# Kernel optimization log

Hardware: AMD Instinct MI355X
Metric: run time of the kernel (lower is better)

## Reference

```python
import jax, jax.numpy as jnp
import numpy as np

PRE_NMS_THRESH = 0.05
PRE_NMS_TOP_N = 1000
NMS_THRESH = 0.6
POST_TOP_N = 100
MIN_SIZE = 0.0


def setup_inputs() -> dict:
    key = jax.random.key(0)
    k1, k2, k3 = jax.random.split(key, 3)
    N, C, H, W = 16, 80, 100, 152
    stride = 8.0
    xs = (jnp.arange(W, dtype=jnp.float32) + 0.5) * stride
    ys = (jnp.arange(H, dtype=jnp.float32) + 0.5) * stride
    yy, xx = jnp.meshgrid(ys, xs, indexing='ij')
    locations = jnp.stack([xx.reshape(-1), yy.reshape(-1)], axis=-1)  # [HW,2] (x,y)
    box_cls = jax.random.normal(k1, (N, C, H, W), jnp.float32) - 2.0  # logits
    box_regression = jax.random.uniform(k2, (N, 4, H, W), jnp.float32) * 64.0  # l,t,r,b >= 0
    centerness = jax.random.normal(k3, (N, 1, H, W), jnp.float32)
    image_sizes = jnp.tile(jnp.array([[800, 1216]], dtype=jnp.int32), (N, 1))  # (h, w)
    return {"locations": locations, "box_cls": box_cls, "box_regression": box_regression,
            "centerness": centerness, "image_sizes": image_sizes}


def _iou_matrix(b):  # b: [K,4] xyxy
    area = (b[:, 2] - b[:, 0]) * (b[:, 3] - b[:, 1])
    lt = jnp.maximum(b[:, None, :2], b[None, :, :2])
    rb = jnp.minimum(b[:, None, 2:], b[None, :, 2:])
    wh = jnp.clip(rb - lt, 0.0)
    inter = wh[..., 0] * wh[..., 1]
    return inter / (area[:, None] + area[None, :] - inter + 1e-9)


def _greedy_nms(iou, valid):  # boxes assumed sorted by score desc
    K = iou.shape[0]
    idx = jnp.arange(K)
    def body(i, sup):
        row = (iou[i] > NMS_THRESH) & (idx > i)
        return jnp.where(sup[i], sup, sup | row)
    sup = jax.lax.fori_loop(0, K, body, ~valid)
    return (~sup) & valid


def _forward(locations, box_cls, box_regression, centerness, image_sizes):
    N, C, H, W = box_cls.shape
    HW = H * W
    cls = jax.nn.sigmoid(jnp.transpose(box_cls, (0, 2, 3, 1)).reshape(N, HW, C))
    reg = jnp.transpose(box_regression, (0, 2, 3, 1)).reshape(N, HW, 4)
    ctr = jax.nn.sigmoid(jnp.transpose(centerness, (0, 2, 3, 1)).reshape(N, HW))
    cand = cls > PRE_NMS_THRESH
    scores = cls * ctr[:, :, None]
    flat = jnp.where(cand, scores, -jnp.inf).reshape(N, HW * C)
    top_scores, top_idx = jax.lax.top_k(flat, PRE_NMS_TOP_N)  # sorted desc
    loc_idx = top_idx // C
    labels = top_idx % C + 1
    valid = top_scores > -jnp.inf
    ar = jnp.arange(N)[:, None]
    reg_k = reg[ar, loc_idx]      # [N,K,4]
    loc_k = locations[loc_idx]    # [N,K,2]
    x1 = loc_k[..., 0] - reg_k[..., 0]
    y1 = loc_k[..., 1] - reg_k[..., 1]
    x2 = loc_k[..., 0] + reg_k[..., 2]
    y2 = loc_k[..., 1] + reg_k[..., 3]
    hi = image_sizes[:, 0:1].astype(x1.dtype)
    wi = image_sizes[:, 1:2].astype(x1.dtype)
    x1 = jnp.clip(x1, 0.0, wi - 1.0); x2 = jnp.clip(x2, 0.0, wi - 1.0)
    y1 = jnp.clip(y1, 0.0, hi - 1.0); y2 = jnp.clip(y2, 0.0, hi - 1.0)
    valid = valid & (x2 - x1 >= MIN_SIZE) & (y2 - y1 >= MIN_SIZE)
    sc = jnp.where(valid, jnp.sqrt(jnp.where(valid, top_scores, 1.0)), 0.0)
    boxes = jnp.stack([x1, y1, x2, y2], axis=-1)  # [N,K,4]
    # multi-class NMS: offset each class into a disjoint coordinate range
    off = labels.astype(x1.dtype) * (jnp.maximum(wi, hi) + 1.0)
    iou = jax.vmap(_iou_matrix)(boxes + off[..., None])  # [N,K,K]
    keep = jax.vmap(_greedy_nms)(iou, valid)
    fscores = jnp.where(keep, sc, -1.0)
    fs, fidx = jax.lax.top_k(fscores, POST_TOP_N)
    fvalid = fs >= 0.0
    boxes_f = boxes[ar, fidx] * fvalid[..., None]
    labels_f = jnp.where(fvalid, labels[ar, fidx], 0)
    dets = jnp.concatenate([boxes_f, jnp.where(fvalid, fs, 0.0)[..., None]], axis=-1)  # [N,100,5]
    return dets, labels_f


def reference(locations, box_cls, box_regression, centerness, image_sizes):
    return _forward(locations, box_cls, box_regression, centerness, image_sizes)
```

## Files before the change

kernel.cpp:

```cpp
#include <hip/hip_runtime.h>
#include <cstdint>

#define NIMG  16
#define NCLS  80
#define HH    100
#define WW    152
#define HWSZ  (HH*WW)
#define HW4   (HWSZ/4)
#define NE    (HWSZ*NCLS)
#define KTOP  1000
#define POSTN 100
#define PRE_T 0.05f
#define NMS_T 0.6f
#define FLOOR_KEY 0x3D000000u
#define FLOOR_BIN 976
#define CAND_CAP  8192
#define SEL_CAP   2048
#define MROWS 16

#define OFF_HIST1 972800u
#define OFF_HIST2 1234944u
#define OFF_META  1497088u
#define OFF_CAND  1498112u
#define OFF_BOX   2546688u
#define OFF_OBOX  2802688u
#define OFF_SC    3058688u
#define OFF_LAB   3122688u
#define OFF_MASK  3186688u

__device__ __forceinline__ float sigm(float x) { return 1.f / (1.f + expf(-x)); }

__device__ __forceinline__ uint64_t shfl64(uint64_t v, int src) {
  int lo = __shfl((int)(uint32_t)(v & 0xffffffffu), src, 64);
  int hi = __shfl((int)(uint32_t)(v >> 32), src, 64);
  return ((uint64_t)(uint32_t)hi << 32) | (uint32_t)lo;
}
__device__ __forceinline__ uint64_t shfl64x(uint64_t v, int d) {
  int lo = __shfl_xor((int)(uint32_t)(v & 0xffffffffu), d, 64);
  int hi = __shfl_xor((int)(uint32_t)(v >> 32), d, 64);
  return ((uint64_t)(uint32_t)hi << 32) | (uint32_t)lo;
}

__device__ __forceinline__ void bitonic_desc_tpp(uint64_t* s, int nn, int t, int nt) {
  const int np = nn >> 1;
  for (int k2 = 2; k2 <= nn; k2 <<= 1) {
    for (int j = k2 >> 1; j > 0; j >>= 1) {
      __syncthreads();
      for (int q = t; q < np; q += nt) {
        int i = ((q & ~(j - 1)) << 1) | (q & (j - 1));
        int p = i | j;
        uint64_t a = s[i], b = s[p];
        bool desc = ((i & k2) == 0);
        bool sw = desc ? (a < b) : (a > b);
        if (sw) { s[i] = b; s[p] = a; }
      }
    }
  }
  __syncthreads();
}

__global__ void k_hist(const float4* __restrict__ cls4, const float4* __restrict__ ctr4,
                       unsigned* __restrict__ hist1) {
  __shared__ unsigned h[4096];
  const int n = blockIdx.y;
  const int z = blockIdx.z;
  for (int i = threadIdx.x; i < 4096; i += blockDim.x) h[i] = 0;
  __syncthreads();
  const int idx = blockIdx.x * blockDim.x + threadIdx.x;
  if (idx < HW4) {
    const float4 c4 = ctr4[n * HW4 + idx];
    const float ct0 = sigm(c4.x), ct1 = sigm(c4.y), ct2 = sigm(c4.z), ct3 = sigm(c4.w);
    const float4* cp = cls4 + (size_t)n * (NE / 4);
#pragma unroll 4
    for (int c = z * 16; c < z * 16 + 16; ++c) {
      float4 v = cp[c * HW4 + idx];
      float s0 = sigm(v.x), s1 = sigm(v.y), s2 = sigm(v.z), s3 = sigm(v.w);
      unsigned k0 = (s0 > PRE_T) ? __float_as_uint(s0 * ct0) : 0u;
      unsigned k1 = (s1 > PRE_T) ? __float_as_uint(s1 * ct1) : 0u;
      unsigned k2 = (s2 > PRE_T) ? __float_as_uint(s2 * ct2) : 0u;
      unsigned k3 = (s3 > PRE_T) ? __float_as_uint(s3 * ct3) : 0u;
      if (k0 >= FLOOR_KEY) atomicAdd(&h[k0 >> 20], 1u);
      if (k1 >= FLOOR_KEY) atomicAdd(&h[k1 >> 20], 1u);
      if (k2 >= FLOOR_KEY) atomicAdd(&h[k2 >> 20], 1u);
      if (k3 >= FLOOR_KEY) atomicAdd(&h[k3 >> 20], 1u);
    }
  }
  __syncthreads();
  for (int i = threadIdx.x; i < 4096; i += blockDim.x) {
    unsigned v = h[i];
    if (v) atomicAdd(&hist1[n * 4096 + i], v);
  }
}

__global__ void k_findbin(const unsigned* __restrict__ hist1, unsigned* __restrict__ meta) {
  const int n = blockIdx.x;
  __shared__ unsigned part[256];
  const unsigned* h = hist1 + n * 4096;
  const int t = threadIdx.x;
  unsigned ps = 0;
  for (int i = 0; i < 16; ++i) ps += h[t * 16 + i];
  part[t] = ps;
  __syncthreads();
  if (t == 0) {
    unsigned cum = 0, cumAbove = 0;
    int bin = -1;
    for (int ch = 255; ch >= 0 && bin < 0; --ch) {
      if (cum + part[ch] >= (unsigned)KTOP) {
        for (int i = 15; i >= 0; --i) {
          unsigned v = h[ch * 16 + i];
          if (cum + v >= (unsigned)KTOP) { bin = ch * 16 + i; cumAbove = cum; break; }
          cum += v;
        }
      } else cum += part[ch];
    }
    if (bin < 0) {
      bin = FLOOR_BIN;
      cumAbove = cum - h[FLOOR_BIN];
    }
    meta[n * 16 + 0] = (unsigned)bin;
    meta[n * 16 + 1] = cumAbove;
  }
}

__global__ void k_collect(const float4* __restrict__ cls4, const float4* __restrict__ ctr4,
                          unsigned* __restrict__ meta, unsigned* __restrict__ hist2,
                          uint64_t* __restrict__ cand) {
  const int n = blockIdx.y;
  const int z = blockIdx.z;
  const unsigned thr1 = meta[n * 16 + 0];
  const unsigned thrKey1 = thr1 << 20;
  const int idx = blockIdx.x * blockDim.x + threadIdx.x;
  if (idx >= HW4) return;
  const float4 c4 = ctr4[n * HW4 + idx];
  const float cc[4] = {sigm(c4.x), sigm(c4.y), sigm(c4.z), sigm(c4.w)};
  const float4* cp = cls4 + (size_t)n * (NE / 4);
  for (int c = z * 16; c < z * 16 + 16; ++c) {
    float4 v = cp[c * HW4 + idx];
    float ss[4] = {sigm(v.x), sigm(v.y), sigm(v.z), sigm(v.w)};
#pragma unroll
    for (int j = 0; j < 4; ++j) {
      unsigned key = (ss[j] > PRE_T) ? __float_as_uint(ss[j] * cc[j]) : 0u;
      if (key >= thrKey1) {
        unsigned fidx = (unsigned)((idx * 4 + j) * NCLS + c);
        uint64_t comp = ((uint64_t)key << 21) | (uint64_t)(0x1FFFFFu - fidx);
        unsigned pos = atomicAdd(&meta[n * 16 + 2], 1u);
        if (pos < CAND_CAP) cand[(size_t)n * CAND_CAP + pos] = comp;
        if ((key >> 20) == thr1) atomicAdd(&hist2[n * 4096 + ((key >> 8) & 0xFFFu)], 1u);
      }
    }
  }
}

__global__ void __launch_bounds__(1024) k_select(
    const unsigned* __restrict__ hist2, unsigned* __restrict__ meta,
    const uint64_t* __restrict__ cand,
    const float* __restrict__ locations, const float* __restrict__ breg,
    const int* __restrict__ imsz,
    float* __restrict__ boxes, float* __restrict__ obox,
    float* __restrict__ scw, int* __restrict__ labw) {
  const int n = blockIdx.x;
  const int t = threadIdx.x;
  __shared__ uint64_t sel[SEL_CAP];
  __shared__ unsigned part[256];
  __shared__ int selcnt;
  __shared__ unsigned thrKey2s;
  const unsigned thr1 = meta[n * 16 + 0];
  const unsigned cumAbove = meta[n * 16 + 1];
  const int ccount = (int)min(meta[n * 16 + 2], (unsigned)CAND_CAP);
  const unsigned* h2 = hist2 + n * 4096;
  if (t < 256) {
    unsigned ps = 0;
    for (int i = 0; i < 16; ++i) ps += h2[t * 16 + i];
    part[t] = ps;
  }
  if (t == 0) selcnt = 0;
  __syncthreads();
  if (t == 0) {
    int need = (int)KTOP - (int)cumAbove;
    unsigned cum = 0;
    int b2 = -1;
    for (int ch = 255; ch >= 0 && b2 < 0; --ch) {
      if ((int)(cum + part[ch]) >= need) {
        for (int i = 15; i >= 0; --i) {
          unsigned v = h2[ch * 16 + i];
          if ((int)(cum + v) >= need) { b2 = ch * 16 + i; break; }
          cum += v;
        }
      } else cum += part[ch];
    }
    thrKey2s = (b2 < 0) ? (thr1 << 20) : ((thr1 << 20) | ((unsigned)b2 << 8));
  }
  __syncthreads();
  const unsigned thrKey2 = thrKey2s;
  for (int j = t; j < ccount; j += 1024) {
    uint64_t comp = cand[(size_t)n * CAND_CAP + j];
    unsigned key = (unsigned)(comp >> 21);
    if (key >= thrKey2) {
      int pos = atomicAdd(&selcnt, 1);
      if (pos < SEL_CAP) sel[pos] = comp;
    }
  }
  __syncthreads();
  const int m = min(selcnt, SEL_CAP);
  for (int j = t + m; j < SEL_CAP; j += 1024) sel[j] = 0;
  __syncthreads();
  bitonic_desc_tpp(sel, SEL_CAP, t, 1024);
  const int nv = min(m, KTOP);
  if (t == 0) meta[n * 16 + 3] = (unsigned)nv;
  const float hi = (float)imsz[n * 2 + 0];
  const float wi = (float)imsz[n * 2 + 1];
  const float offmul = fmaxf(wi, hi) + 1.0f;
  for (int k = t; k < KTOP; k += 1024) {
    float x1 = 0, y1 = 0, x2 = 0, y2 = 0, ox1 = 0, oy1 = 0, ox2 = 0, oy2 = 0, s = 0;
    int lab = 0;
    if (k < nv) {
      uint64_t comp = sel[k];
      unsigned key = (unsigned)(comp >> 21);
      unsigned idx = 0x1FFFFFu - (unsigned)(comp & 0x1FFFFFu);
      int hw = (int)(idx / NCLS);
      int c  = (int)(idx - (unsigned)hw * NCLS);
      lab = c + 1;
      float lx = locations[hw * 2 + 0];
      float ly = locations[hw * 2 + 1];
      const float* rg = breg + (size_t)n * 4 * HWSZ;
      float rl = rg[hw], rt = rg[HWSZ + hw], rr = rg[2 * HWSZ + hw], rb = rg[3 * HWSZ + hw];
      x1 = fminf(fmaxf(lx - rl, 0.f), wi - 1.f);
      x2 = fminf(fmaxf(lx + rr, 0.f), wi - 1.f);
      y1 = fminf(fmaxf(ly - rt, 0.f), hi - 1.f);
      y2 = fminf(fmaxf(ly + rb, 0.f), hi - 1.f);
      float off = (float)lab * offmul;
      asm volatile("" : "+v"(off));
      ox1 = x1 + off; oy1 = y1 + off; ox2 = x2 + off; oy2 = y2 + off;
      s = sqrtf(__uint_as_float(key));
    }
    size_t b = (size_t)(n * KTOP + k);
    boxes[b * 4 + 0] = x1; boxes[b * 4 + 1] = y1; boxes[b * 4 + 2] = x2; boxes[b * 4 + 3] = y2;
    obox[b * 4 + 0] = ox1; obox[b * 4 + 1] = oy1; obox[b * 4 + 2] = ox2; obox[b * 4 + 3] = oy2;
    scw[b] = s;
    labw[b] = lab;
  }
}

__global__ void k_mask(const float* __restrict__ obox, const unsigned* __restrict__ meta,
                       uint64_t* __restrict__ masks) {
  const int n = blockIdx.y;
  const int r0 = blockIdx.x * MROWS;
  const int nv = (int)meta[n * 16 + 3];
  if (r0 >= nv) return;
  __shared__ float4 obs[KTOP];
  __shared__ float ars[KTOP];
  const int t = threadIdx.x;
  const float4* ob = (const float4*)obox + (size_t)n * KTOP;
  for (int j = t; j < KTOP; j += 256) {
    float4 b = ob[j];
    obs[j] = b;
    ars[j] = (b.z - b.x) * (b.w - b.y);
  }
  __syncthreads();
  const int lane = t & 63;
  const int wv = t >> 6;
  for (int rr = wv; rr < MROWS; rr += 4) {
    const int r = r0 + rr;
    if (r >= nv) continue;
    const float4 bi = obs[r];
    const float areai = ars[r];
    uint64_t* mr = masks + ((size_t)n * KTOP + r) * 16;
    for (int w = 0; w < 16; ++w) {
      int j = (w << 6) + lane;
      bool pred = false;
      if (j > r && j < nv) {
        float4 bj = obs[j];
        float areaj = ars[j];
        float ltx = fmaxf(bi.x, bj.x), lty = fmaxf(bi.y, bj.y);
        float rbx = fminf(bi.z, bj.z), rby = fminf(bi.w, bj.w);
        float wx = fmaxf(rbx - ltx, 0.f), wy = fmaxf(rby - lty, 0.f);
        float inter = wx * wy;
        asm volatile("" : "+v"(inter));
        float denom = areai + areaj - inter + 1e-9f;
        pred = (inter / denom) > NMS_T;
      }
      uint64_t bm = __ballot(pred);
      if (lane == 0) mr[w] = bm;
    }
  }
}

#define TSTEP(d, Ld) { uint64_t tp = shfl64x(col, d); \
  col = ((lane & d) == 0) ? ((col & (Ld)) | ((tp & (Ld)) << d)) \
                          : ((col & ~(Ld)) | ((tp & ~(Ld)) >> d)); }

__global__ void __launch_bounds__(1024) k_final(
    const uint64_t* __restrict__ masks, const unsigned* __restrict__ meta,
    const float* __restrict__ boxes, const float* __restrict__ scw,
    const int* __restrict__ labw, float* __restrict__ out) {
  const int n = blockIdx.x;
  const int t = threadIdx.x;
  __shared__ uint64_t shm[KTOP * 16];
  __shared__ uint64_t cols[16 * 64];
  __shared__ uint64_t keepbits[16];
  const int nv = (int)meta[n * 16 + 3];
  const int lane = t & 63;
  const int wv = t >> 6;
  const ulonglong2* src = (const ulonglong2*)(masks + (size_t)n * KTOP * 16);
  ulonglong2* dst = (ulonglong2*)shm;
  for (int j = t; j < KTOP * 8; j += 1024) dst[j] = src[j];
  __syncthreads();
  {
    const int W = wv;
    uint64_t col = shm[(size_t)((W << 6) + lane) * 16 + W];
    TSTEP(32, 0x00000000FFFFFFFFull)
    TSTEP(16, 0x0000FFFF0000FFFFull)
    TSTEP(8,  0x00FF00FF00FF00FFull)
    TSTEP(4,  0x0F0F0F0F0F0F0F0Full)
    TSTEP(2,  0x3333333333333333ull)
    TSTEP(1,  0x5555555555555555ull)
    cols[(W << 6) | lane] = col;
  }
  __syncthreads();
  if (t < 64) {
    uint64_t colr[16];
#pragma unroll
    for (int W = 0; W < 16; ++W) colr[W] = cols[(W << 6) | lane];
    uint64_t rmv = 0;
    const uint64_t below = (lane == 0) ? 0ull : (~0ull >> (64 - lane));
#pragma unroll
    for (int W = 0; W < 16; ++W) {
      const int lo = W << 6;
      uint64_t cur0 = shfl64(rmv, W);
      if (nv <= lo) cur0 = ~0ull;
      else if (nv < lo + 64) cur0 |= (~0ull) << (nv - lo);
      uint64_t kept = ~cur0;
      for (int it = 0; it < 64; ++it) {
        bool pred = (((cur0 >> lane) & 1ull) == 0) && ((colr[W] & kept & below) == 0ull);
        uint64_t kn = __ballot(pred);
        if (kn == kept) break;
        kept = kn;
      }
      if (lane == 0) keepbits[W] = kept;
      const int w = lane & 15, g = lane >> 4;
      uint64_t acc = 0;
#pragma unroll
      for (int i2 = 0; i2 < 16; ++i2) {
        const int i = (i2 << 2) + g;
        uint64_t msk = (uint64_t)0 - ((kept >> i) & 1ull);
        acc |= shm[(size_t)(lo + i) * 16 + w] & msk;
      }
      acc |= shfl64x(acc, 16);
      acc |= shfl64x(acc, 32);
      if (lane < 16) rmv |= acc;
    }
  }
  __syncthreads();
  uint64_t* sel = shm;
  {
    const int k = t;
    uint64_t comp = 0;
    if (k < KTOP && ((keepbits[k >> 6] >> (k & 63)) & 1ull)) {
      unsigned kb = __float_as_uint(scw[(size_t)n * KTOP + k]);
      comp = ((uint64_t)kb << 10) | (uint64_t)(1023 - k);
    }
    sel[k] = comp;
  }
  __syncthreads();
  bitonic_desc_tpp(sel, 1024, t, 1024);
  if (t < POSTN) {
    const int k = t;
    uint64_t comp = sel[k];
    float x1 = 0, y1 = 0, x2 = 0, y2 = 0, fs = 0;
    int lab = 0;
    if (comp != 0) {
      int i = 1023 - (int)(comp & 0x3FFull);
      fs = __uint_as_float((unsigned)(comp >> 10));
      size_t b = (size_t)(n * KTOP + i);
      x1 = boxes[b * 4 + 0]; y1 = boxes[b * 4 + 1]; x2 = boxes[b * 4 + 2]; y2 = boxes[b * 4 + 3];
      lab = labw[b];
    }
    float* dr = out + (size_t)(n * POSTN + k) * 5;
    dr[0] = x1; dr[1] = y1; dr[2] = x2; dr[3] = y2; dr[4] = fs;
    out[(size_t)NIMG * POSTN * 5 + (size_t)n * POSTN + k] = (float)lab;
  }
}

extern "C" void kernel_launch(void* const* d_in, const int* in_sizes, int n_in,
                              void* d_out, int out_size, void* d_ws, size_t ws_size,
                              hipStream_t stream) {
  const float* locations = (const float*)d_in[0];
  const float* box_cls = (const float*)d_in[1];
  const float* box_reg = (const float*)d_in[2];
  const float* centerness = (const float*)d_in[3];
  const int* image_sizes = (const int*)d_in[4];
  char* ws = (char*)d_ws;

  unsigned* hist1 = (unsigned*)(ws + OFF_HIST1);
  unsigned* hist2 = (unsigned*)(ws + OFF_HIST2);
  unsigned* meta = (unsigned*)(ws + OFF_META);
  uint64_t* cand = (uint64_t*)(ws + OFF_CAND);
  float* boxes = (float*)(ws + OFF_BOX);
  float* obox = (float*)(ws + OFF_OBOX);
  float* scw = (float*)(ws + OFF_SC);
  int* labw = (int*)(ws + OFF_LAB);
  uint64_t* masks = (uint64_t*)(ws + OFF_MASK);
  float* out = (float*)d_out;

  hipMemsetAsync(ws + OFF_HIST1, 0, (OFF_META + 1024) - OFF_HIST1, stream);

  k_hist<<<dim3(15, NIMG, 5), 256, 0, stream>>>((const float4*)box_cls,
                                                (const float4*)centerness, hist1);
  k_findbin<<<NIMG, 256, 0, stream>>>(hist1, meta);
  k_collect<<<dim3(15, NIMG, 5), 256, 0, stream>>>((const float4*)box_cls,
                                                   (const float4*)centerness, meta, hist2, cand);
  k_select<<<NIMG, 1024, 0, stream>>>(hist2, meta, cand, locations, box_reg, image_sizes,
                                      boxes, obox, scw, labw);
  k_mask<<<dim3((KTOP + MROWS - 1) / MROWS, NIMG), 256, 0, stream>>>(obox, meta, masks);
  k_final<<<NIMG, 1024, 0, stream>>>(masks, meta, boxes, scw, labw, out);
}
```

Baseline: 159.7 us.

## Skip cold score tiles in collect via per-tile max; split NMS final kernel

The histogram pass now also records the maximum key of each 64-element spatial tile per class. The collect pass reads only tiles whose maximum reaches the threshold bin, instead of re-reading and re-sigmoiding the whole class-logit tensor. The mask kernel now writes the transposed intra-word suppression columns directly, which removes the in-kernel bit transpose. The old final kernel is split into a scan kernel, which uses bank-conflict-padded shared memory, and a separate output/sort kernel. This adds one launch and some scattered global loads in collect.

```diff
diff --git a/kernel.cpp b/kernel.cpp
--- a/kernel.cpp
+++ b/kernel.cpp
@@ -17,6 +17,8 @@
 #define CAND_CAP  8192
 #define SEL_CAP   2048
 #define MROWS 16
+#define NTILE 240
+#define NCHUNK (NCLS*NTILE)
 
 #define OFF_HIST1 972800u
 #define OFF_HIST2 1234944u
@@ -27,6 +29,9 @@
 #define OFF_SC    3058688u
 #define OFF_LAB   3122688u
 #define OFF_MASK  3186688u
+#define OFF_CMAX  2546688u
+#define OFF_COLS  5234688u
+#define OFF_KEEP  5365760u
 
 __device__ __forceinline__ float sigm(float x) { return 1.f / (1.f + expf(-x)); }
 
@@ -60,33 +65,45 @@
 }
 
 __global__ void k_hist(const float4* __restrict__ cls4, const float4* __restrict__ ctr4,
-                       unsigned* __restrict__ hist1) {
+                       unsigned* __restrict__ hist1, unsigned* __restrict__ cmax) {
   __shared__ unsigned h[4096];
   const int n = blockIdx.y;
   const int z = blockIdx.z;
-  for (int i = threadIdx.x; i < 4096; i += blockDim.x) h[i] = 0;
-  __syncthreads();
-  const int idx = blockIdx.x * blockDim.x + threadIdx.x;
+  const int t = threadIdx.x;
+  for (int i = t; i < 4096; i += blockDim.x) h[i] = 0;
+  __syncthreads();
+  const int idx = blockIdx.x * blockDim.x + t;
+  float ct0 = 0, ct1 = 0, ct2 = 0, ct3 = 0;
   if (idx < HW4) {
     const float4 c4 = ctr4[n * HW4 + idx];
-    const float ct0 = sigm(c4.x), ct1 = sigm(c4.y), ct2 = sigm(c4.z), ct3 = sigm(c4.w);
-    const float4* cp = cls4 + (size_t)n * (NE / 4);
+    ct0 = sigm(c4.x); ct1 = sigm(c4.y); ct2 = sigm(c4.z); ct3 = sigm(c4.w);
+  }
+  const float4* cp = cls4 + (size_t)n * (NE / 4);
+  const int tile = idx >> 4;
 #pragma unroll 4
-    for (int c = z * 16; c < z * 16 + 16; ++c) {
+  for (int c = z * 16; c < z * 16 + 16; ++c) {
+    unsigned k0 = 0, k1 = 0, k2 = 0, k3 = 0;
+    if (idx < HW4) {
       float4 v = cp[c * HW4 + idx];
       float s0 = sigm(v.x), s1 = sigm(v.y), s2 = sigm(v.z), s3 = sigm(v.w);
-      unsigned k0 = (s0 > PRE_T) ? __float_as_uint(s0 * ct0) : 0u;
-      unsigned k1 = (s1 > PRE_T) ? __float_as_uint(s1 * ct1) : 0u;
-      unsigned k2 = (s2 > PRE_T) ? __float_as_uint(s2 * ct2) : 0u;
-      unsigned k3 = (s3 > PRE_T) ? __float_as_uint(s3 * ct3) : 0u;
+      k0 = (s0 > PRE_T) ? __float_as_uint(s0 * ct0) : 0u;
+      k1 = (s1 > PRE_T) ? __float_as_uint(s1 * ct1) : 0u;
+      k2 = (s2 > PRE_T) ? __float_as_uint(s2 * ct2) : 0u;
+      k3 = (s3 > PRE_T) ? __float_as_uint(s3 * ct3) : 0u;
       if (k0 >= FLOOR_KEY) atomicAdd(&h[k0 >> 20], 1u);
       if (k1 >= FLOOR_KEY) atomicAdd(&h[k1 >> 20], 1u);
       if (k2 >= FLOOR_KEY) atomicAdd(&h[k2 >> 20], 1u);
       if (k3 >= FLOOR_KEY) atomicAdd(&h[k3 >> 20], 1u);
     }
-  }
-  __syncthreads();
-  for (int i = threadIdx.x; i < 4096; i += blockDim.x) {
+    unsigned km = max(max(k0, k1), max(k2, k3));
+    km = max(km, (unsigned)__shfl_xor((int)km, 1, 64));
+    km = max(km, (unsigned)__shfl_xor((int)km, 2, 64));
+    km = max(km, (unsigned)__shfl_xor((int)km, 4, 64));
+    km = max(km, (unsigned)__shfl_xor((int)km, 8, 64));
+    if ((t & 15) == 0) cmax[(size_t)n * NCHUNK + c * NTILE + tile] = km;
+  }
+  __syncthreads();
+  for (int i = t; i < 4096; i += blockDim.x) {
     unsigned v = h[i];
     if (v) atomicAdd(&hist1[n * 4096 + i], v);
   }
@@ -122,26 +139,29 @@
   }
 }
 
-__global__ void k_collect(const float4* __restrict__ cls4, const float4* __restrict__ ctr4,
+__global__ void k_collect(const float* __restrict__ cls, const float* __restrict__ ctr,
+                          const unsigned* __restrict__ cmax,
                           unsigned* __restrict__ meta, unsigned* __restrict__ hist2,
                           uint64_t* __restrict__ cand) {
   const int n = blockIdx.y;
-  const int z = blockIdx.z;
   const unsigned thr1 = meta[n * 16 + 0];
   const unsigned thrKey1 = thr1 << 20;
-  const int idx = blockIdx.x * blockDim.x + threadIdx.x;
-  if (idx >= HW4) return;
-  const float4 c4 = ctr4[n * HW4 + idx];
-  const float cc[4] = {sigm(c4.x), sigm(c4.y), sigm(c4.z), sigm(c4.w)};
-  const float4* cp = cls4 + (size_t)n * (NE / 4);
-  for (int c = z * 16; c < z * 16 + 16; ++c) {
-    float4 v = cp[c * HW4 + idx];
-    float ss[4] = {sigm(v.x), sigm(v.y), sigm(v.z), sigm(v.w)};
-#pragma unroll
-    for (int j = 0; j < 4; ++j) {
-      unsigned key = (ss[j] > PRE_T) ? __float_as_uint(ss[j] * cc[j]) : 0u;
+  const int lane = threadIdx.x & 63;
+  const int cbase = (blockIdx.x * 4 + (threadIdx.x >> 6)) * 64;
+  unsigned cm = cmax[(size_t)n * NCHUNK + cbase + lane];
+  uint64_t hot = __ballot(cm >= thrKey1);
+  while (hot) {
+    int b = __ffsll((unsigned long long)hot) - 1;
+    hot &= hot - 1;
+    int hc = cbase + b;
+    int c = hc / NTILE, tile = hc - c * NTILE;
+    int hw = tile * 64 + lane;
+    if (hw < HWSZ) {
+      float s1 = sigm(cls[((size_t)n * NCLS + c) * HWSZ + hw]);
+      float sc = sigm(ctr[(size_t)n * HWSZ + hw]);
+      unsigned key = (s1 > PRE_T) ? __float_as_uint(s1 * sc) : 0u;
       if (key >= thrKey1) {
-        unsigned fidx = (unsigned)((idx * 4 + j) * NCLS + c);
+        unsigned fidx = (unsigned)(hw * NCLS + c);
         uint64_t comp = ((uint64_t)key << 21) | (uint64_t)(0x1FFFFFu - fidx);
         unsigned pos = atomicAdd(&meta[n * 16 + 2], 1u);
         if (pos < CAND_CAP) cand[(size_t)n * CAND_CAP + pos] = comp;
@@ -242,7 +262,7 @@
 }
 
 __global__ void k_mask(const float* __restrict__ obox, const unsigned* __restrict__ meta,
-                       uint64_t* __restrict__ masks) {
+                       uint64_t* __restrict__ masks, uint64_t* __restrict__ colsg) {
   const int n = blockIdx.y;
   const int r0 = blockIdx.x * MROWS;
   const int nv = (int)meta[n * 16 + 3];
@@ -264,11 +284,12 @@
     if (r >= nv) continue;
     const float4 bi = obs[r];
     const float areai = ars[r];
+    const int Wr = r >> 6;
     uint64_t* mr = masks + ((size_t)n * KTOP + r) * 16;
     for (int w = 0; w < 16; ++w) {
       int j = (w << 6) + lane;
-      bool pred = false;
-      if (j > r && j < nv) {
+      bool over = false;
+      if (j < nv && j != r) {
         float4 bj = obs[j];
         float areaj = ars[j];
         float ltx = fmaxf(bi.x, bj.x), lty = fmaxf(bi.y, bj.y);
@@ -277,50 +298,38 @@
         float inter = wx * wy;
         asm volatile("" : "+v"(inter));
         float denom = areai + areaj - inter + 1e-9f;
-        pred = (inter / denom) > NMS_T;
-      }
-      uint64_t bm = __ballot(pred);
-      if (lane == 0) mr[w] = bm;
-    }
-  }
-}
-
-#define TSTEP(d, Ld) { uint64_t tp = shfl64x(col, d); \
-  col = ((lane & d) == 0) ? ((col & (Ld)) | ((tp & (Ld)) << d)) \
-                          : ((col & ~(Ld)) | ((tp & ~(Ld)) >> d)); }
-
-__global__ void __launch_bounds__(1024) k_final(
-    const uint64_t* __restrict__ masks, const unsigned* __restrict__ meta,
-    const float* __restrict__ boxes, const float* __restrict__ scw,
-    const int* __restrict__ labw, float* __restrict__ out) {
+        over = (inter / denom) > NMS_T;
+      }
+      uint64_t bu = __ballot(over && (j > r));
+      if (lane == 0) mr[w] = bu;
+      if (w == Wr) {
+        uint64_t bc = __ballot(over && (j < r));
+        if (lane == 0) colsg[((size_t)n * 16 + w) * 64 + (r & 63)] = bc;
+      }
+    }
+  }
+}
+
+__global__ void __launch_bounds__(1024) k_scan(
+    const uint64_t* __restrict__ masks, const uint64_t* __restrict__ colsg,
+    const unsigned* __restrict__ meta, uint64_t* __restrict__ keep_g) {
   const int n = blockIdx.x;
   const int t = threadIdx.x;
-  __shared__ uint64_t shm[KTOP * 16];
-  __shared__ uint64_t cols[16 * 64];
-  __shared__ uint64_t keepbits[16];
+  __shared__ uint64_t shmP[KTOP * 17];
   const int nv = (int)meta[n * 16 + 3];
   const int lane = t & 63;
-  const int wv = t >> 6;
   const ulonglong2* src = (const ulonglong2*)(masks + (size_t)n * KTOP * 16);
-  ulonglong2* dst = (ulonglong2*)shm;
-  for (int j = t; j < KTOP * 8; j += 1024) dst[j] = src[j];
-  __syncthreads();
-  {
-    const int W = wv;
-    uint64_t col = shm[(size_t)((W << 6) + lane) * 16 + W];
-    TSTEP(32, 0x00000000FFFFFFFFull)
-    TSTEP(16, 0x0000FFFF0000FFFFull)
-    TSTEP(8,  0x00FF00FF00FF00FFull)
-    TSTEP(4,  0x0F0F0F0F0F0F0F0Full)
-    TSTEP(2,  0x3333333333333333ull)
-    TSTEP(1,  0x5555555555555555ull)
-    cols[(W << 6) | lane] = col;
+  for (int j2 = t; j2 < KTOP * 8; j2 += 1024) {
+    ulonglong2 v = src[j2];
+    int row = j2 >> 3, wp = (j2 & 7) << 1;
+    shmP[row * 17 + wp] = v.x;
+    shmP[row * 17 + wp + 1] = v.y;
   }
   __syncthreads();
   if (t < 64) {
     uint64_t colr[16];
 #pragma unroll
-    for (int W = 0; W < 16; ++W) colr[W] = cols[(W << 6) | lane];
+    for (int W = 0; W < 16; ++W) colr[W] = colsg[((size_t)n * 16 + W) * 64 + lane];
     uint64_t rmv = 0;
     const uint64_t below = (lane == 0) ? 0ull : (~0ull >> (64 - lane));
 #pragma unroll
@@ -336,28 +345,38 @@
         if (kn == kept) break;
         kept = kn;
       }
-      if (lane == 0) keepbits[W] = kept;
+      if (lane == 0) keep_g[n * 16 + W] = kept;
       const int w = lane & 15, g = lane >> 4;
       uint64_t acc = 0;
 #pragma unroll
       for (int i2 = 0; i2 < 16; ++i2) {
         const int i = (i2 << 2) + g;
         uint64_t msk = (uint64_t)0 - ((kept >> i) & 1ull);
-        acc |= shm[(size_t)(lo + i) * 16 + w] & msk;
+        acc |= shmP[(lo + i) * 17 + w] & msk;
       }
       acc |= shfl64x(acc, 16);
       acc |= shfl64x(acc, 32);
       if (lane < 16) rmv |= acc;
     }
   }
-  __syncthreads();
-  uint64_t* sel = shm;
+}
+
+__global__ void __launch_bounds__(1024) k_out(
+    const uint64_t* __restrict__ keep_g, const float* __restrict__ boxes,
+    const float* __restrict__ scw, const int* __restrict__ labw,
+    float* __restrict__ out) {
+  const int n = blockIdx.x;
+  const int t = threadIdx.x;
+  __shared__ uint64_t sel[1024];
+  __shared__ uint64_t kb[16];
+  if (t < 16) kb[t] = keep_g[n * 16 + t];
+  __syncthreads();
   {
     const int k = t;
     uint64_t comp = 0;
-    if (k < KTOP && ((keepbits[k >> 6] >> (k & 63)) & 1ull)) {
-      unsigned kb = __float_as_uint(scw[(size_t)n * KTOP + k]);
-      comp = ((uint64_t)kb << 10) | (uint64_t)(1023 - k);
+    if (k < KTOP && ((kb[k >> 6] >> (k & 63)) & 1ull)) {
+      unsigned s = __float_as_uint(scw[(size_t)n * KTOP + k]);
+      comp = ((uint64_t)s << 10) | (uint64_t)(1023 - k);
     }
     sel[k] = comp;
   }
@@ -400,17 +419,21 @@
   float* scw = (float*)(ws + OFF_SC);
   int* labw = (int*)(ws + OFF_LAB);
   uint64_t* masks = (uint64_t*)(ws + OFF_MASK);
+  unsigned* cmaxp = (unsigned*)(ws + OFF_CMAX);
+  uint64_t* colsg = (uint64_t*)(ws + OFF_COLS);
+  uint64_t* keep_g = (uint64_t*)(ws + OFF_KEEP);
   float* out = (float*)d_out;
 
   hipMemsetAsync(ws + OFF_HIST1, 0, (OFF_META + 1024) - OFF_HIST1, stream);
 
   k_hist<<<dim3(15, NIMG, 5), 256, 0, stream>>>((const float4*)box_cls,
-                                                (const float4*)centerness, hist1);
+                                                (const float4*)centerness, hist1, cmaxp);
   k_findbin<<<NIMG, 256, 0, stream>>>(hist1, meta);
-  k_collect<<<dim3(15, NIMG, 5), 256, 0, stream>>>((const float4*)box_cls,
-                                                   (const float4*)centerness, meta, hist2, cand);
+  k_collect<<<dim3(75, NIMG), 256, 0, stream>>>(box_cls, centerness, cmaxp,
+                                                meta, hist2, cand);
   k_select<<<NIMG, 1024, 0, stream>>>(hist2, meta, cand, locations, box_reg, image_sizes,
                                       boxes, obox, scw, labw);
-  k_mask<<<dim3((KTOP + MROWS - 1) / MROWS, NIMG), 256, 0, stream>>>(obox, meta, masks);
-  k_final<<<NIMG, 1024, 0, stream>>>(masks, meta, boxes, scw, labw, out);
-}
+  k_mask<<<dim3((KTOP + MROWS - 1) / MROWS, NIMG), 256, 0, stream>>>(obox, meta, masks, colsg);
+  k_scan<<<NIMG, 1024, 0, stream>>>(masks, colsg, meta, keep_g);
+  k_out<<<NIMG, 1024, 0, stream>>>(keep_g, boxes, scw, labw, out);
+}
```

After: 170.3 us. 6.6% more time.
